# Kernel optimization log

Measured on AMD Instinct MI355X. Metric: run time of the kernel, lower is better.

Reference implementation:

```python
import jax, jax.numpy as jnp
import numpy as np

ALPHA = 1.5
BETA = 45.0
LAMDA = 0.5
B = 8192   # batch_size
D = 128    # feature dim (hardcoded in original via zeros((1,128)))
V = 4      # number of views stacked in fj
EPS = 1e-12  # F.normalize eps


def _l2norm_rows(x):
    n = jnp.sqrt(jnp.sum(x * x, axis=-1, keepdims=True))
    return x / jnp.maximum(n, EPS)


def setup_inputs() -> dict:
    key = jax.random.key(0)
    k1, k2 = jax.random.split(key)
    fi = jax.random.normal(k1, (B, D), dtype=jnp.float32)
    fj = jax.random.normal(k2, (V, B, D), dtype=jnp.float32)
    # L2-normalize embeddings so exp(beta*(SVM - lamda)) stays finite (beta=45)
    fi = _l2norm_rows(fi)
    fj = _l2norm_rows(fj)
    return {"fi": fi, "fj": fj, "b": V}


def avg_svm(fi, fj):
    # Original: per-row softmax-weighted average of fj rows, renormalized,
    # dotted with fi row, averaged over the batch.
    A = fi @ fj.T                      # [B, B] pairwise logits
    W = jax.nn.softmax(A, axis=1)      # softmax over j (alphalist / sumofalpha)
    Vw = W @ fj                        # [B, D] softmax-weighted averages
    Vn = _l2norm_rows(Vw)              # F.normalize(p=2, dim=1)
    return jnp.mean(jnp.sum(fi * Vn, axis=1))  # mean_i fi[i] . Vn[i]


def reference(fi, fj, b):
    b = int(b)
    # SMM1 is recomputed identically every outer iteration in the original;
    # compute once and multiply the per-iteration term by (b-1).
    smm1 = avg_svm(fi, fi)
    if b > 2:
        # inner loop: SMM2sum is a running (cumulative) sum over j=1..b-2,
        # and exp(beta*(SMM2sum - lamda)) is added at every step.
        s_vals = jnp.stack([avg_svm(fi, fj[j]) for j in range(1, b - 1)])
        cum = jnp.cumsum(s_vals)
        ssum = jnp.sum(jnp.exp(BETA * (cum - LAMDA)))
    else:
        ssum = jnp.exp(BETA * (avg_svm(fi, fj) - LAMDA))
    term = (1.0 / ALPHA) * jnp.log1p(jnp.exp(-ALPHA * (smm1 - LAMDA))) \
         + (1.0 / BETA) * jnp.log1p(ssum)
    loss = (b - 1) * term
    return jnp.squeeze(loss)
```

## Files before the change

### kernel.cpp

```cpp
#include <hip/hip_runtime.h>

#define BDIM 8192
#define DDIM 128

typedef __attribute__((ext_vector_type(4))) float floatx4;
typedef __attribute__((ext_vector_type(4))) int   intx4;
typedef __attribute__((ext_vector_type(8))) int   intx8;

#define SLAB (BDIM * DDIM)
#define G8_OFF 64
#define G8T_OFF (64 + 3 * SLAB)

__device__ inline intx8 ld_pair(const char* base, int c0) {
    union { intx8 v; intx4 h[2]; } u;
    u.h[0] = *(const intx4*)(base + c0 * 16);
    u.h[1] = *(const intx4*)(base + (c0 ^ 1) * 16);
    return u.v;
}

__device__ inline float exp_fast(float x) {
    return __builtin_amdgcn_exp2f(x * 1.44269504088896341f);
}

__global__ __launch_bounds__(256)
void prep_kernel(const float* __restrict__ fi, const float* __restrict__ fj,
                 unsigned char* __restrict__ g8, unsigned char* __restrict__ g8T,
                 float* __restrict__ acc)
{
    const int p = blockIdx.y;
    const int kblock = blockIdx.x;
    const int rbase = kblock * 32;
    const int tid = threadIdx.x;
    if (p == 0 && kblock == 0 && tid < 8) acc[tid] = 0.f;
    const float* src = (p == 0) ? fi : (fj + (size_t)p * SLAB);

    __shared__ __align__(16) unsigned char T8[32][144];

    {
        const int row = tid >> 3, c = tid & 7;
        const float* sp = src + (size_t)(rbase + row) * DDIM + c * 16;
        float4 f0 = ((const float4*)sp)[0];
        float4 f1 = ((const float4*)sp)[1];
        float4 f2 = ((const float4*)sp)[2];
        float4 f3 = ((const float4*)sp)[3];
        alignas(16) int w[4];
        w[0] = __builtin_amdgcn_cvt_pk_fp8_f32(f0.x, f0.y, 0, false);
        w[0] = __builtin_amdgcn_cvt_pk_fp8_f32(f0.z, f0.w, w[0], true);
        w[1] = __builtin_amdgcn_cvt_pk_fp8_f32(f1.x, f1.y, 0, false);
        w[1] = __builtin_amdgcn_cvt_pk_fp8_f32(f1.z, f1.w, w[1], true);
        w[2] = __builtin_amdgcn_cvt_pk_fp8_f32(f2.x, f2.y, 0, false);
        w[2] = __builtin_amdgcn_cvt_pk_fp8_f32(f2.z, f2.w, w[2], true);
        w[3] = __builtin_amdgcn_cvt_pk_fp8_f32(f3.x, f3.y, 0, false);
        w[3] = __builtin_amdgcn_cvt_pk_fp8_f32(f3.z, f3.w, w[3], true);
        int4 v = *(int4*)w;
        *(int4*)(g8 + (size_t)p * SLAB + (size_t)(rbase + row) * DDIM + c * 16) = v;
        *(int4*)(&T8[row][c * 16]) = v;
    }
    __syncthreads();
    {
        const int d = tid >> 1, half = tid & 1;
        alignas(16) unsigned char bb[16];
        #pragma unroll
        for (int i = 0; i < 16; ++i) bb[i] = T8[half * 16 + i][d];
        *(int4*)(g8T + (size_t)p * SLAB + (size_t)kblock * 4096 + d * 32 + half * 16) =
            *(int4*)bb;
    }
}

__global__ __launch_bounds__(256, 3)
void flash_kernel(const float* __restrict__ fi,
                  const unsigned char* __restrict__ g8,
                  const unsigned char* __restrict__ g8T,
                  float* __restrict__ acc)
{
    const int b = blockIdx.x;
    const int gp = (b & 7) * 96 + (b >> 3);
    const int p = gp >> 8;
    const int qbase = (gp & 255) * 32;
    const int tid = threadIdx.x;
    const int wave = tid >> 6, lane = tid & 63;
    const int quad = lane >> 4, col = lane & 15;

    __shared__ __align__(16) char smem[8192];
    #define POFF 0

    const unsigned char* g8p  = g8  + (size_t)p * SLAB;
    const unsigned char* g8Tp = g8T + (size_t)p * SLAB;

    intx8 qf[2];
    #pragma unroll
    for (int qt = 0; qt < 2; ++qt) {
        const intx4* qp = (const intx4*)(g8 + (size_t)(qbase + qt * 16 + col) * DDIM +
                                         quad * 32);
        union { intx8 v; intx4 h[2]; } u;
        u.h[0] = qp[0];
        u.h[1] = qp[1];
        qf[qt] = u.v;
    }

    floatx4 O[2][2];
    #pragma unroll
    for (int qt = 0; qt < 2; ++qt)
        #pragma unroll
        for (int j = 0; j < 2; ++j)
            O[qt][j] = (floatx4){0.f, 0.f, 0.f, 0.f};

    const unsigned char* pK0 = g8p + (size_t)(wave * 32 + col) * DDIM + quad * 32;
    const unsigned char* pK1 = pK0 + 16 * DDIM;
    const unsigned char* pV0 = g8Tp + (size_t)quad * 4096 +
                               (size_t)(wave * 2 * 16 + col) * 32;
    const unsigned char* pV1 = pV0 + 16 * 32;

    intx8 kA0, kA1, vA0, vA1, kB0, kB1, vB0, vB1;

#define LOADT(K0, K1, V0, V1)                                          \
    do {                                                               \
        K0 = *(const intx8*)pK0; K1 = *(const intx8*)pK1;              \
        V0 = *(const intx8*)pV0; V1 = *(const intx8*)pV1;              \
        pK0 += 16384; pK1 += 16384; pV0 += 16384; pV1 += 16384;        \
    } while (0)

    auto half_iter = [&](int k, intx8 kf0, intx8 kf1, intx8 vf0, intx8 vf1) {
        floatx4 S[2][2];
        __builtin_amdgcn_s_setprio(1);
        S[0][0] = __builtin_amdgcn_mfma_scale_f32_16x16x128_f8f6f4(
            kf0, qf[0], (floatx4){0.f, 0.f, 0.f, 0.f}, 0, 0, 0, 127, 0, 127);
        S[0][1] = __builtin_amdgcn_mfma_scale_f32_16x16x128_f8f6f4(
            kf0, qf[1], (floatx4){0.f, 0.f, 0.f, 0.f}, 0, 0, 0, 127, 0, 127);
        S[1][0] = __builtin_amdgcn_mfma_scale_f32_16x16x128_f8f6f4(
            kf1, qf[0], (floatx4){0.f, 0.f, 0.f, 0.f}, 0, 0, 0, 127, 0, 127);
        S[1][1] = __builtin_amdgcn_mfma_scale_f32_16x16x128_f8f6f4(
            kf1, qf[1], (floatx4){0.f, 0.f, 0.f, 0.f}, 0, 0, 0, 127, 0, 127);
        __builtin_amdgcn_s_setprio(0);

        char* pw = smem + POFF + ((k & 1) << 12);
        #pragma unroll
        for (int kt = 0; kt < 2; ++kt)
            #pragma unroll
            for (int qt = 0; qt < 2; ++qt) {
                int v = __builtin_amdgcn_cvt_pk_fp8_f32(
                    exp_fast(S[kt][qt][0]), exp_fast(S[kt][qt][1]), 0, false);
                v = __builtin_amdgcn_cvt_pk_fp8_f32(
                    exp_fast(S[kt][qt][2]), exp_fast(S[kt][qt][3]), v, true);
                const int q = qt * 16 + col;
                *(int*)(pw + q * 128 +
                        (((wave * 2 + kt) ^ (q & 7)) << 4) + quad * 4) = v;
            }

        asm volatile("s_waitcnt lgkmcnt(0)\n\ts_barrier" ::: "memory");

        const char* pr = smem + POFF + ((k & 1) << 12);
        __builtin_amdgcn_s_setprio(1);
        #pragma unroll
        for (int qt = 0; qt < 2; ++qt) {
            const int q = qt * 16 + col;
            intx8 pf = ld_pair(pr + q * 128, (quad * 2) ^ (q & 7));
            O[qt][0] = __builtin_amdgcn_mfma_scale_f32_16x16x128_f8f6f4(
                pf, vf0, O[qt][0], 0, 0, 0, 127, 0, 127);
            O[qt][1] = __builtin_amdgcn_mfma_scale_f32_16x16x128_f8f6f4(
                pf, vf1, O[qt][1], 0, 0, 0, 127, 0, 127);
        }
        __builtin_amdgcn_s_setprio(0);
    };

    LOADT(kA0, kA1, vA0, vA1);

    for (int k = 0; k < 64; k += 2) {
        LOADT(kB0, kB1, vB0, vB1);
        half_iter(k, kA0, kA1, vA0, vA1);
        if (k + 2 < 64) LOADT(kA0, kA1, vA0, vA1);
        half_iter(k + 1, kB0, kB1, vB0, vB1);
    }

    float* pdot = (float*)(smem + POFF);
    float* pnrm = (float*)(smem + POFF + 512);
    #pragma unroll
    for (int qt = 0; qt < 2; ++qt)
        #pragma unroll
        for (int r = 0; r < 4; ++r) {
            const int q = qt * 16 + quad * 4 + r;
            float dot = 0.f, nr = 0.f;
            #pragma unroll
            for (int j = 0; j < 2; ++j) {
                float o = O[qt][j][r];
                float fq = fi[(size_t)(qbase + q) * DDIM + (wave * 2 + j) * 16 + col];
                dot += fq * o;
                nr += o * o;
            }
            #pragma unroll
            for (int m = 1; m < 16; m <<= 1) {
                dot += __shfl_xor(dot, m, 64);
                nr  += __shfl_xor(nr,  m, 64);
            }
            if (col == 0) {
                pdot[wave * 32 + q] = dot;
                pnrm[wave * 32 + q] = nr;
            }
        }
    __syncthreads();
    if (tid < 32) {
        const int q = tid;
        float D = pdot[q] + pdot[32 + q] + pdot[64 + q] + pdot[96 + q];
        float N = pnrm[q] + pnrm[32 + q] + pnrm[64 + q] + pnrm[96 + q];
        float val = D * rsqrtf(fmaxf(N, 1e-30f));
        #pragma unroll
        for (int m = 1; m < 32; m <<= 1) val += __shfl_xor(val, m, 64);
        if (tid == 0) atomicAdd(&acc[p], val);
    }
}

__global__ void final_kernel(const float* __restrict__ acc, float* __restrict__ out)
{
    if (threadIdx.x == 0 && blockIdx.x == 0) {
        const double s0 = (double)acc[0] / (double)BDIM;
        const double s1 = (double)acc[1] / (double)BDIM;
        const double s2 = (double)acc[2] / (double)BDIM;
        const double t1 = (1.0 / 1.5) * log1p(exp(-1.5 * (s0 - 0.5)));
        const double ssum = exp(45.0 * (s1 - 0.5)) + exp(45.0 * (s1 + s2 - 0.5));
        const double t2 = (1.0 / 45.0) * log1p(ssum);
        out[0] = (float)(3.0 * (t1 + t2));
    }
}

extern "C" void kernel_launch(void* const* d_in, const int* in_sizes, int n_in,
                              void* d_out, int out_size, void* d_ws, size_t ws_size,
                              hipStream_t stream)
{
    const float* fi = (const float*)d_in[0];
    const float* fj = (const float*)d_in[1];

    float* acc = (float*)d_ws;
    unsigned char* g8  = (unsigned char*)d_ws + G8_OFF;
    unsigned char* g8T = (unsigned char*)d_ws + G8T_OFF;

    prep_kernel <<<dim3(BDIM / 32, 3), 256, 0, stream>>>(fi, fj, g8, g8T, acc);
    flash_kernel<<<dim3(768), 256, 0, stream>>>(fi, g8, g8T, acc);
    final_kernel<<<1, 64, 0, stream>>>(acc, (float*)d_out);
}
```

Before: 189.3 us.

## Stage K/V tiles via direct-to-LDS loads and split keys across waves

The flash kernel now copies K and V tiles straight into shared memory with global_load_lds, and each wave handles its own key subset across the full 128-wide output. This removes the per-step P exchange through shared memory and the block barrier inside the key loop. P stays in registers and feeds 16x16x32 fp8 MFMAs over 8 output tiles. Partial outputs are then reduced across waves in shared memory at the end. The prep kernel's transposed V layout is swizzled to match the new read pattern. In exchange, shared memory grows to about 49 KB and accumulator registers rise, which may lower occupancy, and the single-stage load/wait gives less overlap.

Result: faster. 155.1 us (-18.0%).

```diff
diff --git a/kernel.cpp b/kernel.cpp
--- a/kernel.cpp
+++ b/kernel.cpp
@@ -6,10 +6,17 @@
 typedef __attribute__((ext_vector_type(4))) float floatx4;
 typedef __attribute__((ext_vector_type(4))) int   intx4;
 typedef __attribute__((ext_vector_type(8))) int   intx8;
+typedef long i64;
 
 #define SLAB (BDIM * DDIM)
 #define G8_OFF 64
 #define G8T_OFF (64 + 3 * SLAB)
+
+__device__ inline void load_lds16(const void* g, void* l) {
+    __builtin_amdgcn_global_load_lds(
+        (const __attribute__((address_space(1))) unsigned int*)g,
+        (__attribute__((address_space(3))) unsigned int*)l, 16, 0, 0);
+}
 
 __device__ inline intx8 ld_pair(const char* base, int c0) {
     union { intx8 v; intx4 h[2]; } u;
@@ -59,9 +66,15 @@
     __syncthreads();
     {
         const int d = tid >> 1, half = tid & 1;
+        const int s = (d >> 2) & 3;
         alignas(16) unsigned char bb[16];
         #pragma unroll
-        for (int i = 0; i < 16; ++i) bb[i] = T8[half * 16 + i][d];
+        for (int x = 0; x < 16; ++x) {
+            int g  = (half << 1) + (x >> 3);
+            int u  = x & 7;
+            int kl = ((g ^ s) << 2) + (u & 3) + ((u >> 2) << 4);
+            bb[x] = T8[kl][d];
+        }
         *(int4*)(g8T + (size_t)p * SLAB + (size_t)kblock * 4096 + d * 32 + half * 16) =
             *(int4*)bb;
     }
@@ -81,8 +94,11 @@
     const int wave = tid >> 6, lane = tid & 63;
     const int quad = lane >> 4, col = lane & 15;
 
-    __shared__ __align__(16) char smem[8192];
-    #define POFF 0
+    __shared__ __align__(16) char smem[49792];
+    #define KOFF 0
+    #define VOFF 16384
+    #define OOFF 32768
+    #define PVOFF 49664
 
     const unsigned char* g8p  = g8  + (size_t)p * SLAB;
     const unsigned char* g8Tp = g8T + (size_t)p * SLAB;
@@ -98,114 +114,132 @@
         qf[qt] = u.v;
     }
 
-    floatx4 O[2][2];
+    floatx4 O[2][8];
     #pragma unroll
     for (int qt = 0; qt < 2; ++qt)
         #pragma unroll
-        for (int j = 0; j < 2; ++j)
-            O[qt][j] = (floatx4){0.f, 0.f, 0.f, 0.f};
-
-    const unsigned char* pK0 = g8p + (size_t)(wave * 32 + col) * DDIM + quad * 32;
-    const unsigned char* pK1 = pK0 + 16 * DDIM;
-    const unsigned char* pV0 = g8Tp + (size_t)quad * 4096 +
-                               (size_t)(wave * 2 * 16 + col) * 32;
-    const unsigned char* pV1 = pV0 + 16 * 32;
-
-    intx8 kA0, kA1, vA0, vA1, kB0, kB1, vB0, vB1;
-
-#define LOADT(K0, K1, V0, V1)                                          \
-    do {                                                               \
-        K0 = *(const intx8*)pK0; K1 = *(const intx8*)pK1;              \
-        V0 = *(const intx8*)pV0; V1 = *(const intx8*)pV1;              \
-        pK0 += 16384; pK1 += 16384; pV0 += 16384; pV1 += 16384;        \
-    } while (0)
-
-    auto half_iter = [&](int k, intx8 kf0, intx8 kf1, intx8 vf0, intx8 vf1) {
+        for (int dt = 0; dt < 8; ++dt)
+            O[qt][dt] = (floatx4){0.f, 0.f, 0.f, 0.f};
+
+    const unsigned char* kSrc = g8p + (size_t)wave * 4096 +
+        (size_t)(lane >> 3) * 128 + (size_t)(((lane & 7) ^ ((lane >> 3) & 7)) * 16);
+    const unsigned char* vSrc = g8Tp + (size_t)wave * 4096 + (size_t)lane * 16;
+
+    auto stage = [&]() {
+        #pragma unroll
+        for (int i = 0; i < 4; ++i)
+            load_lds16(kSrc + i * 1024, smem + KOFF + wave * 4096 + i * 1024);
+        #pragma unroll
+        for (int i = 0; i < 4; ++i)
+            load_lds16(vSrc + i * 1024, smem + VOFF + wave * 4096 + i * 1024);
+        kSrc += 16384;
+        vSrc += 16384;
+    };
+
+    const char* kb0 = smem + KOFF + wave * 4096 + col * 128;
+    const char* kb1 = smem + KOFF + wave * 4096 + (16 + col) * 128;
+    const int   kc  = (quad * 2) ^ (col & 7);
+    const char* vbase = smem + VOFF + wave * 4096 + col * 32 +
+                        ((quad ^ (col >> 2)) * 8);
+
+    stage();
+
+    for (int k = 0; k < 64; ++k) {
+        asm volatile("s_waitcnt vmcnt(0)" ::: "memory");
+
+        intx8 kf0 = ld_pair(kb0, kc);
+        intx8 kf1 = ld_pair(kb1, kc);
+        i64 vf[8];
+        #pragma unroll
+        for (int dt = 0; dt < 8; ++dt)
+            vf[dt] = *(const i64*)(vbase + dt * 512);
+
+        asm volatile("s_waitcnt lgkmcnt(0)" ::: "memory");
+        if (k < 63) stage();
+
         floatx4 S[2][2];
         __builtin_amdgcn_s_setprio(1);
         S[0][0] = __builtin_amdgcn_mfma_scale_f32_16x16x128_f8f6f4(
-            kf0, qf[0], (floatx4){0.f, 0.f, 0.f, 0.f}, 0, 0, 0, 127, 0, 127);
+            kf0, qf[0], (floatx4){0.f,0.f,0.f,0.f}, 0, 0, 0, 127, 0, 127);
         S[0][1] = __builtin_amdgcn_mfma_scale_f32_16x16x128_f8f6f4(
-            kf0, qf[1], (floatx4){0.f, 0.f, 0.f, 0.f}, 0, 0, 0, 127, 0, 127);
+            kf0, qf[1], (floatx4){0.f,0.f,0.f,0.f}, 0, 0, 0, 127, 0, 127);
         S[1][0] = __builtin_amdgcn_mfma_scale_f32_16x16x128_f8f6f4(
-            kf1, qf[0], (floatx4){0.f, 0.f, 0.f, 0.f}, 0, 0, 0, 127, 0, 127);
+            kf1, qf[0], (floatx4){0.f,0.f,0.f,0.f}, 0, 0, 0, 127, 0, 127);
         S[1][1] = __builtin_amdgcn_mfma_scale_f32_16x16x128_f8f6f4(
-            kf1, qf[1], (floatx4){0.f, 0.f, 0.f, 0.f}, 0, 0, 0, 127, 0, 127);
+            kf1, qf[1], (floatx4){0.f,0.f,0.f,0.f}, 0, 0, 0, 127, 0, 127);
         __builtin_amdgcn_s_setprio(0);
 
-        char* pw = smem + POFF + ((k & 1) << 12);
-        #pragma unroll
-        for (int kt = 0; kt < 2; ++kt)
+        i64 pf[2];
+        #pragma unroll
+        for (int qt = 0; qt < 2; ++qt) {
+            int w0 = __builtin_amdgcn_cvt_pk_fp8_f32(
+                exp_fast(S[0][qt][0]), exp_fast(S[0][qt][1]), 0, false);
+            w0 = __builtin_amdgcn_cvt_pk_fp8_f32(
+                exp_fast(S[0][qt][2]), exp_fast(S[0][qt][3]), w0, true);
+            int w1 = __builtin_amdgcn_cvt_pk_fp8_f32(
+                exp_fast(S[1][qt][0]), exp_fast(S[1][qt][1]), 0, false);
+            w1 = __builtin_amdgcn_cvt_pk_fp8_f32(
+                exp_fast(S[1][qt][2]), exp_fast(S[1][qt][3]), w1, true);
+            union { i64 l; int i[2]; } u;
+            u.i[0] = w0;
+            u.i[1] = w1;
+            pf[qt] = u.l;
+        }
+
+        __builtin_amdgcn_s_setprio(1);
+        #pragma unroll
+        for (int qt = 0; qt < 2; ++qt)
             #pragma unroll
-            for (int qt = 0; qt < 2; ++qt) {
-                int v = __builtin_amdgcn_cvt_pk_fp8_f32(
-                    exp_fast(S[kt][qt][0]), exp_fast(S[kt][qt][1]), 0, false);
-                v = __builtin_amdgcn_cvt_pk_fp8_f32(
-                    exp_fast(S[kt][qt][2]), exp_fast(S[kt][qt][3]), v, true);
-                const int q = qt * 16 + col;
-                *(int*)(pw + q * 128 +
-                        (((wave * 2 + kt) ^ (q & 7)) << 4) + quad * 4) = v;
-            }
-
-        asm volatile("s_waitcnt lgkmcnt(0)\n\ts_barrier" ::: "memory");
-
-        const char* pr = smem + POFF + ((k & 1) << 12);
-        __builtin_amdgcn_s_setprio(1);
-        #pragma unroll
-        for (int qt = 0; qt < 2; ++qt) {
-            const int q = qt * 16 + col;
-            intx8 pf = ld_pair(pr + q * 128, (quad * 2) ^ (q & 7));
-            O[qt][0] = __builtin_amdgcn_mfma_scale_f32_16x16x128_f8f6f4(
-                pf, vf0, O[qt][0], 0, 0, 0, 127, 0, 127);
-            O[qt][1] = __builtin_amdgcn_mfma_scale_f32_16x16x128_f8f6f4(
-                pf, vf1, O[qt][1], 0, 0, 0, 127, 0, 127);
-        }
+            for (int dt = 0; dt < 8; ++dt)
+                O[qt][dt] = __builtin_amdgcn_mfma_f32_16x16x32_fp8_fp8(
+                    pf[qt], vf[dt], O[qt][dt], 0, 0, 0);
         __builtin_amdgcn_s_setprio(0);
-    };
-
-    LOADT(kA0, kA1, vA0, vA1);
-
-    for (int k = 0; k < 64; k += 2) {
-        LOADT(kB0, kB1, vB0, vB1);
-        half_iter(k, kA0, kA1, vA0, vA1);
-        if (k + 2 < 64) LOADT(kA0, kA1, vA0, vA1);
-        half_iter(k + 1, kB0, kB1, vB0, vB1);
-    }
-
-    float* pdot = (float*)(smem + POFF);
-    float* pnrm = (float*)(smem + POFF + 512);
-    #pragma unroll
-    for (int qt = 0; qt < 2; ++qt)
-        #pragma unroll
-        for (int r = 0; r < 4; ++r) {
-            const int q = qt * 16 + quad * 4 + r;
-            float dot = 0.f, nr = 0.f;
+    }
+
+    float* OL = (float*)(smem + OOFF);
+    #pragma unroll 1
+    for (int w = 0; w < 4; ++w) {
+        if (wave == w) {
             #pragma unroll
-            for (int j = 0; j < 2; ++j) {
-                float o = O[qt][j][r];
-                float fq = fi[(size_t)(qbase + q) * DDIM + (wave * 2 + j) * 16 + col];
-                dot += fq * o;
-                nr += o * o;
-            }
+            for (int qt = 0; qt < 2; ++qt)
+                #pragma unroll
+                for (int dt = 0; dt < 8; ++dt)
+                    #pragma unroll
+                    for (int r = 0; r < 4; ++r) {
+                        const int q = qt * 16 + quad * 4 + r;
+                        const int d = dt * 16 + col;
+                        if (w == 0) OL[q * 132 + d]  = O[qt][dt][r];
+                        else        OL[q * 132 + d] += O[qt][dt][r];
+                    }
+        }
+        __syncthreads();
+    }
+
+    {
+        const int q = tid >> 3, dc = (tid & 7) * 16;
+        const float* fq = fi + (size_t)(qbase + q) * DDIM + dc;
+        float dot = 0.f, nr = 0.f;
+        #pragma unroll
+        for (int u = 0; u < 16; ++u) {
+            float o = OL[q * 132 + dc + u];
+            dot += fq[u] * o;
+            nr  += o * o;
+        }
+        #pragma unroll
+        for (int m = 1; m < 8; m <<= 1) {
+            dot += __shfl_xor(dot, m, 64);
+            nr  += __shfl_xor(nr,  m, 64);
+        }
+        float* pv = (float*)(smem + PVOFF);
+        if ((tid & 7) == 0)
+            pv[q] = dot * rsqrtf(fmaxf(nr, 1e-30f));
+        __syncthreads();
+        if (tid < 32) {
+            float val = pv[tid];
             #pragma unroll
-            for (int m = 1; m < 16; m <<= 1) {
-                dot += __shfl_xor(dot, m, 64);
-                nr  += __shfl_xor(nr,  m, 64);
-            }
-            if (col == 0) {
-                pdot[wave * 32 + q] = dot;
-                pnrm[wave * 32 + q] = nr;
-            }
-        }
-    __syncthreads();
-    if (tid < 32) {
-        const int q = tid;
-        float D = pdot[q] + pdot[32 + q] + pdot[64 + q] + pdot[96 + q];
-        float N = pnrm[q] + pnrm[32 + q] + pnrm[64 + q] + pnrm[96 + q];
-        float val = D * rsqrtf(fmaxf(N, 1e-30f));
-        #pragma unroll
-        for (int m = 1; m < 32; m <<= 1) val += __shfl_xor(val, m, 64);
-        if (tid == 0) atomicAdd(&acc[p], val);
+            for (int m = 1; m < 32; m <<= 1) val += __shfl_xor(val, m, 64);
+            if (tid == 0) atomicAdd(&acc[p], val);
+        }
     }
 }
 
```
